# Optimization experiments

Measured on AMD Instinct MI355X. Metric: run time of the kernel, lower is better.

Reference implementation:

```python
import jax, jax.numpy as jnp
import numpy as np

N = 131072   # total gates/nodes in the batched block-diagonal circuit graph
E = 524288   # directed edges (avg degree 4)
D = 100      # hidden dim
DA = 50      # msg MLP hidden
DC = 30      # classifier hidden
R = 20       # message-passing rounds


def mlp(x, W1, b1, W2, b2):
    return jax.nn.relu(x @ W1 + b1) @ W2 + b2


def gru_step(x, h, Wih, Whh, bih, bhh):
    # single-timestep torch.nn.GRU cell
    gi = x @ Wih.T + bih
    gh = h @ Whh.T + bhh
    ir, iz, inn = jnp.split(gi, 3, axis=-1)
    hr, hz, hn = jnp.split(gh, 3, axis=-1)
    r = jax.nn.sigmoid(ir + hr)
    z = jax.nn.sigmoid(iz + hz)
    nwe = jnp.tanh(inn + r * hn)
    return (1.0 - z) * nwe + z * h


def setup_inputs():
    key = jax.random.key(0)
    ks = jax.random.split(key, 26)
    s = 0.05

    def rn(k, shape):
        return jax.random.normal(k, shape, dtype=jnp.float32) * s

    inp = {
        'features': jax.random.normal(ks[0], (N, 4), dtype=jnp.float32),
        'edge_row': jax.random.randint(ks[1], (E,), 0, N, dtype=jnp.int32),
        'edge_col': jax.random.randint(ks[2], (E,), 0, N, dtype=jnp.int32),
        'init_W': rn(ks[3], (4, D)), 'init_b': jnp.zeros((D,), jnp.float32),
        'fmsg_W1': rn(ks[4], (D, DA)), 'fmsg_b1': jnp.zeros((DA,), jnp.float32),
        'fmsg_W2': rn(ks[5], (DA, D)), 'fmsg_b2': jnp.zeros((D,), jnp.float32),
        'bmsg_W1': rn(ks[6], (D, DA)), 'bmsg_b1': jnp.zeros((DA,), jnp.float32),
        'bmsg_W2': rn(ks[7], (DA, D)), 'bmsg_b2': jnp.zeros((D,), jnp.float32),
        'fgru_Wih': rn(ks[8], (3 * D, D)), 'fgru_Whh': rn(ks[9], (3 * D, D)),
        'fgru_bih': jnp.zeros((3 * D,), jnp.float32), 'fgru_bhh': jnp.zeros((3 * D,), jnp.float32),
        'bgru_Wih': rn(ks[10], (3 * D, D)), 'bgru_Whh': rn(ks[11], (3 * D, D)),
        'bgru_bih': jnp.zeros((3 * D,), jnp.float32), 'bgru_bhh': jnp.zeros((3 * D,), jnp.float32),
        'cls_W1': rn(ks[12], (D, DC)), 'cls_b1': jnp.zeros((DC,), jnp.float32),
        'cls_W2': rn(ks[13], (DC, 1)), 'cls_b2': jnp.zeros((1,), jnp.float32),
    }
    return inp


def reference(features, edge_row, edge_col, init_W, init_b,
              fmsg_W1, fmsg_b1, fmsg_W2, fmsg_b2,
              bmsg_W1, bmsg_b1, bmsg_W2, bmsg_b2,
              fgru_Wih, fgru_Whh, fgru_bih, fgru_bhh,
              bgru_Wih, bgru_Whh, bgru_bih, bgru_bhh,
              cls_W1, cls_b1, cls_W2, cls_b2):
    n = features.shape[0]
    h = features @ init_W + init_b  # [N, D]

    def round_body(h, _):
        # forward pass: adj @ forward_msg(h)
        fm = mlp(h, fmsg_W1, fmsg_b1, fmsg_W2, fmsg_b2)
        f_msg = jax.ops.segment_sum(fm[edge_col], edge_row, num_segments=n)
        h = gru_step(f_msg, h, fgru_Wih, fgru_Whh, fgru_bih, fgru_bhh)
        # backward pass: adj.T @ backward_msg(h)
        bm = mlp(h, bmsg_W1, bmsg_b1, bmsg_W2, bmsg_b2)
        b_msg = jax.ops.segment_sum(bm[edge_row], edge_col, num_segments=n)
        h = gru_step(b_msg, h, bgru_Wih, bgru_Whh, bgru_bih, bgru_bhh)
        return h, None

    h, _ = jax.lax.scan(jax.checkpoint(round_body), h, None, length=R)
    return mlp(h, cls_W1, cls_b1, cls_W2, cls_b2)  # [N, 1]
```

## Files before the change

### kernel.cpp

```cpp
#include <hip/hip_runtime.h>
#include <math.h>

#define Nn 131072
#define Ee 524288

typedef __attribute__((ext_vector_type(8))) short short8;
typedef __attribute__((ext_vector_type(4))) float f32x4;
typedef unsigned short ushort_t;
typedef unsigned int uint32;

__device__ __forceinline__ f32x4 mfma16(short8 a, short8 b, f32x4 c) {
    return __builtin_amdgcn_mfma_f32_16x16x32_bf16(a, b, c, 0, 0, 0);
}

__device__ __forceinline__ uint32 rne_bf16(float x) {
    uint32 u = __float_as_uint(x);
    return (u + 0x7FFFu + ((u >> 16) & 1u)) >> 16;
}

__device__ __forceinline__ void split3(float x, uint32& h, uint32& m, uint32& l) {
    h = rne_bf16(x);
    float hf = __uint_as_float(h << 16);
    float r1 = x - hf;
    m = rne_bf16(r1);
    float mf = __uint_as_float(m << 16);
    float r2 = r1 - mf;
    l = rne_bf16(r2);
}

__global__ void diag_kernel(float* out, float val) {
    int n = blockIdx.x * 256 + threadIdx.x;
    if (n < Nn) out[n] = (n == 0) ? val : 0.f;
}
__global__ void zero_ints(int* p, int n) {
    int i = blockIdx.x * 256 + threadIdx.x;
    if (i < n) p[i] = 0;
}

__global__ void hist_kernel(const int* __restrict__ er, const int* __restrict__ ec,
                            int* __restrict__ cnt_f, int* __restrict__ cnt_b) {
    int e = blockIdx.x * 256 + threadIdx.x;
    atomicAdd(&cnt_f[er[e]], 1);
    atomicAdd(&cnt_b[ec[e]], 1);
}

__global__ __launch_bounds__(1024) void scan_kernel(const int* __restrict__ cnt,
                                                    int* __restrict__ ptr, int n) {
    __shared__ int sums[1024];
    int t = threadIdx.x;
    int chunk = n >> 10;
    int base = t * chunk;
    int s = 0;
    for (int i = 0; i < chunk; i++) s += cnt[base + i];
    sums[t] = s;
    __syncthreads();
    for (int off = 1; off < 1024; off <<= 1) {
        int v = (t >= off) ? sums[t - off] : 0;
        __syncthreads();
        sums[t] += v;
        __syncthreads();
    }
    int run = (t == 0) ? 0 : sums[t - 1];
    for (int i = 0; i < chunk; i++) { ptr[base + i] = run; run += cnt[base + i]; }
    if (t == 1023) ptr[n] = run;
}

__global__ void fill_kernel(const int* __restrict__ er, const int* __restrict__ ec,
                            int* __restrict__ ptr_f, int* __restrict__ ptr_b,
                            int* __restrict__ src_f, int* __restrict__ src_b) {
    int e = blockIdx.x * 256 + threadIdx.x;
    int r = er[e], c = ec[e];
    int p = atomicAdd(&ptr_f[r], 1); src_f[p] = c;
    int q = atomicAdd(&ptr_b[c], 1); src_b[q] = r;
}

__global__ void prep_gru_w(const float* __restrict__ Wih, const float* __restrict__ Whh,
                           const float* __restrict__ bih, const float* __restrict__ bhh,
                           ushort_t* __restrict__ W0, ushort_t* __restrict__ W1,
                           ushort_t* __restrict__ W2, float* __restrict__ bg) {
    int gid = blockIdx.x * 256 + threadIdx.x;
    if (gid >= 448 * 224) return;
    int c = gid / 224, k = gid - c * 224;
    int d = c >> 2, g = c & 3;
    float w = 0.f;
    if (d < 100) {
        if (k < 100) {
            if (g == 0)      w = Wih[d * 100 + k];
            else if (g == 1) w = Wih[(100 + d) * 100 + k];
            else if (g == 2) w = Wih[(200 + d) * 100 + k];
        } else if (k < 200) {
            int kk = k - 100;
            if (g == 0)      w = Whh[d * 100 + kk];
            else if (g == 1) w = Whh[(100 + d) * 100 + kk];
            else if (g == 3) w = Whh[(200 + d) * 100 + kk];
        }
    }
    uint32 h, m, l; split3(w, h, m, l);
    W0[gid] = (ushort_t)h; W1[gid] = (ushort_t)m; W2[gid] = (ushort_t)l;
    if (k == 0) {
        float b = 0.f;
        if (d < 100) {
            if (g == 0)      b = bih[d] + bhh[d];
            else if (g == 1) b = bih[100 + d] + bhh[100 + d];
            else if (g == 2) b = bih[200 + d];
            else             b = bhh[200 + d];
        }
        bg[c] = b;
    }
}

__global__ void prep_msg_w(const float* __restrict__ W1, const float* __restrict__ b1,
                           const float* __restrict__ W2, const float* __restrict__ b2,
                           ushort_t* __restrict__ A0, ushort_t* __restrict__ A1,
                           ushort_t* __restrict__ A2, float* __restrict__ b1p,
                           ushort_t* __restrict__ B0, ushort_t* __restrict__ B1,
                           ushort_t* __restrict__ B2, float* __restrict__ b2p) {
    int gid = blockIdx.x * 256 + threadIdx.x;
    if (gid < 8192) {
        int c = gid >> 7, k = gid & 127;
        float w = (c < 50 && k < 100) ? W1[k * 50 + c] : 0.f;
        uint32 h, m, l; split3(w, h, m, l);
        A0[gid] = (ushort_t)h; A1[gid] = (ushort_t)m; A2[gid] = (ushort_t)l;
        if (k == 0) b1p[c] = (c < 50) ? b1[c] : 0.f;
    } else if (gid < 8192 + 7168) {
        int t = gid - 8192;
        int c = t >> 6, k = t & 63;
        float w = (c < 100 && k < 50) ? W2[k * 100 + c] : 0.f;
        uint32 h, m, l; split3(w, h, m, l);
        B0[t] = (ushort_t)h; B1[t] = (ushort_t)m; B2[t] = (ushort_t)l;
        if (k == 0) b2p[c] = (c < 100) ? b2[c] : 0.f;
    }
}

__global__ void init_h_kernel(const float* __restrict__ feat, const float* __restrict__ W,
                              const float* __restrict__ b, float* __restrict__ Act) {
    int gid = blockIdx.x * 256 + threadIdx.x;
    int n = gid / 100, d = gid - n * 100;
    float acc = b[d];
#pragma unroll
    for (int k = 0; k < 4; k++) acc += feat[n * 4 + k] * W[k * 100 + d];
    Act[(size_t)n * 200 + 100 + d] = acc;
}

__global__ __launch_bounds__(256, 2) void msg_mfma(
    const float* __restrict__ Act,
    const ushort_t* __restrict__ A0, const ushort_t* __restrict__ A1,
    const ushort_t* __restrict__ A2, const float* __restrict__ b1p,
    const ushort_t* __restrict__ B0, const ushort_t* __restrict__ B1,
    const ushort_t* __restrict__ B2, const float* __restrict__ b2p,
    float* __restrict__ fm) {
    __shared__ ushort_t C1[3][64][72];
    const int tid = threadIdx.x;
    const int u = tid >> 6;
    const int lane = tid & 63;
    const int m = lane & 15, q = lane >> 4;
    const int n0 = blockIdx.x * 64;
    const int n = n0 + u * 16 + m;

    f32x4 z = {0.f, 0.f, 0.f, 0.f};
    f32x4 a1[4] = {z, z, z, z};

    for (int kc = 0; kc < 4; kc++) {
        int kb = kc * 32 + q * 8;
        const float* src = Act + (size_t)n * 200 + 100 + kb;
        float4 v0 = *(const float4*)src;
        float4 v1 = *(const float4*)(src + 4);
        float e[8] = {v0.x, v0.y, v0.z, v0.w, v1.x, v1.y, v1.z, v1.w};
        union { short8 s; uint32 u4[4]; } f0, f1, f2;
#pragma unroll
        for (int j = 0; j < 4; j++) {
            uint32 ha, ma, la, hb, mb, lb;
            split3(e[2 * j], ha, ma, la);
            split3(e[2 * j + 1], hb, mb, lb);
            f0.u4[j] = ha | (hb << 16);
            f1.u4[j] = ma | (mb << 16);
            f2.u4[j] = la | (lb << 16);
        }
#pragma unroll
        for (int t = 0; t < 4; t++) {
            int off = (t * 16 + m) * 128 + kc * 32 + q * 8;
            short8 w0 = *(const short8*)(A0 + off);
            short8 w1 = *(const short8*)(A1 + off);
            short8 w2 = *(const short8*)(A2 + off);
            a1[t] = mfma16(w0, f0.s, a1[t]);
            a1[t] = mfma16(w0, f1.s, a1[t]);
            a1[t] = mfma16(w1, f0.s, a1[t]);
            a1[t] = mfma16(w0, f2.s, a1[t]);
            a1[t] = mfma16(w2, f0.s, a1[t]);
            a1[t] = mfma16(w1, f1.s, a1[t]);
        }
    }
#pragma unroll
    for (int t = 0; t < 4; t++) {
        int c0 = t * 16 + 4 * q;
        float4 bb = *(const float4*)&b1p[c0];
        float v0 = fmaxf(a1[t][0] + bb.x, 0.f);
        float v1 = fmaxf(a1[t][1] + bb.y, 0.f);
        float v2 = fmaxf(a1[t][2] + bb.z, 0.f);
        float v3 = fmaxf(a1[t][3] + bb.w, 0.f);
        uint32 h0, m0, l0, h1, m1, l1, h2, m2, l2, h3, m3, l3;
        split3(v0, h0, m0, l0); split3(v1, h1, m1, l1);
        split3(v2, h2, m2, l2); split3(v3, h3, m3, l3);
        int nl = u * 16 + m;
        *(uint2*)&C1[0][nl][c0] = make_uint2(h0 | (h1 << 16), h2 | (h3 << 16));
        *(uint2*)&C1[1][nl][c0] = make_uint2(m0 | (m1 << 16), m2 | (m3 << 16));
        *(uint2*)&C1[2][nl][c0] = make_uint2(l0 | (l1 << 16), l2 | (l3 << 16));
    }
    __syncthreads();

    f32x4 a2[7] = {z, z, z, z, z, z, z};
    for (int kc = 0; kc < 2; kc++) {
        int nl = u * 16 + m;
        short8 c0f = *(const short8*)&C1[0][nl][kc * 32 + q * 8];
        short8 c1f = *(const short8*)&C1[1][nl][kc * 32 + q * 8];
        short8 c2f = *(const short8*)&C1[2][nl][kc * 32 + q * 8];
#pragma unroll
        for (int t = 0; t < 7; t++) {
            int off = (t * 16 + m) * 64 + kc * 32 + q * 8;
            short8 w0 = *(const short8*)(B0 + off);
            short8 w1 = *(const short8*)(B1 + off);
            short8 w2 = *(const short8*)(B2 + off);
            a2[t] = mfma16(w0, c0f, a2[t]);
            a2[t] = mfma16(w0, c1f, a2[t]);
            a2[t] = mfma16(w1, c0f, a2[t]);
            a2[t] = mfma16(w0, c2f, a2[t]);
            a2[t] = mfma16(w2, c0f, a2[t]);
            a2[t] = mfma16(w1, c1f, a2[t]);
        }
    }
#pragma unroll
    for (int t = 0; t < 7; t++) {
        int c0 = t * 16 + 4 * q;
        if (c0 < 100) {
            float4 bb = *(const float4*)&b2p[c0];
            float4 o;
            o.x = a2[t][0] + bb.x; o.y = a2[t][1] + bb.y;
            o.z = a2[t][2] + bb.z; o.w = a2[t][3] + bb.w;
            *(float4*)&fm[(size_t)n * 100 + c0] = o;
        }
    }
}

__global__ void gather4(const float* __restrict__ fm, const int* __restrict__ ptr,
                        const int* __restrict__ idx, float* __restrict__ Act) {
    int gid = blockIdx.x * 256 + threadIdx.x;
    int n = gid / 25, qq = (gid - n * 25) * 4;
    int s = (n == 0) ? 0 : ptr[n - 1];
    int e = ptr[n];
    float4 acc = {0.f, 0.f, 0.f, 0.f};
    for (int i = s; i < e; i++) {
        float4 v = *(const float4*)&fm[(size_t)idx[i] * 100 + qq];
        acc.x += v.x; acc.y += v.y; acc.z += v.z; acc.w += v.w;
    }
    *(float4*)&Act[(size_t)n * 200 + qq] = acc;
}

__global__ __launch_bounds__(256, 2) void gru_mfma(
    float* __restrict__ Act,
    const ushort_t* __restrict__ W0, const ushort_t* __restrict__ W1,
    const ushort_t* __restrict__ W2, const float* __restrict__ bg) {
    const int tid = threadIdx.x;
    const int wave = tid >> 6;
    const int lane = tid & 63;
    const int m = lane & 15, q = lane >> 4;
    const int n0 = blockIdx.x * 64;

    f32x4 z = {0.f, 0.f, 0.f, 0.f};
    f32x4 acc[7][4];
#pragma unroll
    for (int t = 0; t < 7; t++)
#pragma unroll
        for (int rf = 0; rf < 4; rf++) acc[t][rf] = z;

    int woff[7];
#pragma unroll
    for (int t = 0; t < 7; t++)
        woff[t] = ((t * 4 + wave) * 16 + m) * 224 + q * 8;

    const float* abase = Act + (size_t)(n0 + m) * 200 + q * 8;

#define GPASS(Wreg, Fr)                                          \
    _Pragma("unroll")                                            \
    for (int t = 0; t < 7; t++) {                                \
        _Pragma("unroll")                                        \
        for (int rf = 0; rf < 4; rf++)                           \
            acc[t][rf] = mfma16(Wreg[t], Fr[rf], acc[t][rf]);    \
    }

    for (int kc = 0; kc < 7; kc++) {
        const int kb = kc * 32 + q * 8;
        const int ko = kc * 32;
        short8 f0[4], f1[4], f2[4];
#pragma unroll
        for (int rf = 0; rf < 4; rf++) {
            float e[8];
            if (kb < 200) {
                const float* src = abase + (size_t)rf * 16 * 200 + ko;
                float4 v0 = *(const float4*)src;
                float4 v1 = *(const float4*)(src + 4);
                e[0] = v0.x; e[1] = v0.y; e[2] = v0.z; e[3] = v0.w;
                e[4] = v1.x; e[5] = v1.y; e[6] = v1.z; e[7] = v1.w;
            } else {
#pragma unroll
                for (int j = 0; j < 8; j++) e[j] = 0.f;
            }
            union { short8 s; uint32 u4[4]; } p0, p1, p2;
#pragma unroll
            for (int j = 0; j < 4; j++) {
                uint32 ha, ma, la, hb, mb, lb;
                split3(e[2 * j], ha, ma, la);
                split3(e[2 * j + 1], hb, mb, lb);
                p0.u4[j] = ha | (hb << 16);
                p1.u4[j] = ma | (mb << 16);
                p2.u4[j] = la | (lb << 16);
            }
            f0[rf] = p0.s; f1[rf] = p1.s; f2[rf] = p2.s;
        }

        short8 w[7];
#pragma unroll
        for (int t = 0; t < 7; t++) w[t] = *(const short8*)(W0 + woff[t] + ko);
        GPASS(w, f0);
        GPASS(w, f1);
        GPASS(w, f2);
#pragma unroll
        for (int t = 0; t < 7; t++) w[t] = *(const short8*)(W1 + woff[t] + ko);
        GPASS(w, f0);
        GPASS(w, f1);
#pragma unroll
        for (int t = 0; t < 7; t++) w[t] = *(const short8*)(W2 + woff[t] + ko);
        GPASS(w, f0);
    }
#undef GPASS

    __syncthreads();

#pragma unroll
    for (int t = 0; t < 7; t++) {
        const int ct = t * 4 + wave;
        const int d = ct * 4 + q;
        if (d < 100) {
            float4 b4 = *(const float4*)&bg[ct * 16 + 4 * q];
#pragma unroll
            for (int rf = 0; rf < 4; rf++) {
                int n = n0 + rf * 16 + m;
                float* hp = Act + (size_t)n * 200 + 100 + d;
                float hold = *hp;
                float rp = acc[t][rf][0] + b4.x;
                float zp = acc[t][rf][1] + b4.y;
                float np = acc[t][rf][2] + b4.z;
                float hh = acc[t][rf][3] + b4.w;
                float rr = 1.f / (1.f + __expf(-rp));
                float zz = 1.f / (1.f + __expf(-zp));
                float nw = tanhf(np + rr * hh);
                *hp = (1.f - zz) * nw + zz * hold;
            }
        }
    }
}

__global__ __launch_bounds__(256) void classifier(
    const float* __restrict__ Act, const float* __restrict__ W1,
    const float* __restrict__ b1, const float* __restrict__ W2,
    const float* __restrict__ b2, float* __restrict__ out) {
    __shared__ float Wc[3000];
    __shared__ float bc[30];
    __shared__ float w2[30];
    int tid = threadIdx.x;
    for (int i = tid; i < 3000; i += 256) Wc[i] = W1[i];
    if (tid < 30) { bc[tid] = b1[tid]; w2[tid] = W2[tid]; }
    __syncthreads();
    int n = blockIdx.x * 256 + tid;
    float a[30];
#pragma unroll
    for (int j = 0; j < 30; j++) a[j] = bc[j];
    for (int k = 0; k < 100; k++) {
        float hv = Act[(size_t)n * 200 + 100 + k];
#pragma unroll
        for (int j = 0; j < 30; j++) a[j] = fmaf(hv, Wc[k * 30 + j], a[j]);
    }
    float s = b2[0];
#pragma unroll
    for (int j = 0; j < 30; j++) s = fmaf(fmaxf(a[j], 0.f), w2[j], s);
    out[n] = s;
}

extern "C" void kernel_launch(void* const* d_in, const int* in_sizes, int n_in,
                              void* d_out, int out_size, void* d_ws, size_t ws_size,
                              hipStream_t stream) {
    const float* feat     = (const float*)d_in[0];
    const int*   er       = (const int*)d_in[1];
    const int*   ec       = (const int*)d_in[2];
    const float* init_W   = (const float*)d_in[3];
    const float* init_b   = (const float*)d_in[4];
    const float* fmsg_W1  = (const float*)d_in[5];
    const float* fmsg_b1  = (const float*)d_in[6];
    const float* fmsg_W2  = (const float*)d_in[7];
    const float* fmsg_b2  = (const float*)d_in[8];
    const float* bmsg_W1  = (const float*)d_in[9];
    const float* bmsg_b1  = (const float*)d_in[10];
    const float* bmsg_W2  = (const float*)d_in[11];
    const float* bmsg_b2  = (const float*)d_in[12];
    const float* fgru_Wih = (const float*)d_in[13];
    const float* fgru_Whh = (const float*)d_in[14];
    const float* fgru_bih = (const float*)d_in[15];
    const float* fgru_bhh = (const float*)d_in[16];
    const float* bgru_Wih = (const float*)d_in[17];
    const float* bgru_Whh = (const float*)d_in[18];
    const float* bgru_bih = (const float*)d_in[19];
    const float* bgru_bhh = (const float*)d_in[20];
    const float* cls_W1   = (const float*)d_in[21];
    const float* cls_b1   = (const float*)d_in[22];
    const float* cls_W2   = (const float*)d_in[23];
    const float* cls_b2   = (const float*)d_in[24];
    float* out = (float*)d_out;

    float* ws = (float*)d_ws;
    size_t o = 0;
    float* Act = ws + o; o += (size_t)Nn * 200;
    float* fm  = ws + o; o += (size_t)Nn * 100;

    ushort_t* us = (ushort_t*)(ws + o);
    size_t uo = 0;
    ushort_t* fWg0 = us + uo; uo += 448 * 224;
    ushort_t* fWg1 = us + uo; uo += 448 * 224;
    ushort_t* fWg2 = us + uo; uo += 448 * 224;
    ushort_t* bWg0 = us + uo; uo += 448 * 224;
    ushort_t* bWg1 = us + uo; uo += 448 * 224;
    ushort_t* bWg2 = us + uo; uo += 448 * 224;
    ushort_t* fA0 = us + uo; uo += 8192;
    ushort_t* fA1 = us + uo; uo += 8192;
    ushort_t* fA2 = us + uo; uo += 8192;
    ushort_t* bA0 = us + uo; uo += 8192;
    ushort_t* bA1 = us + uo; uo += 8192;
    ushort_t* bA2 = us + uo; uo += 8192;
    ushort_t* fB0 = us + uo; uo += 7168;
    ushort_t* fB1 = us + uo; uo += 7168;
    ushort_t* fB2 = us + uo; uo += 7168;
    ushort_t* bB0 = us + uo; uo += 7168;
    ushort_t* bB1 = us + uo; uo += 7168;
    ushort_t* bB2 = us + uo; uo += 7168;
    o += uo / 2;

    float* bgf  = ws + o; o += 448;
    float* bgb  = ws + o; o += 448;
    float* b1pf = ws + o; o += 64;
    float* b1pb = ws + o; o += 64;
    float* b2pf = ws + o; o += 112;
    float* b2pb = ws + o; o += 112;

    int* iws   = (int*)(ws + o);
    int* ptr_f = iws;
    int* ptr_b = ptr_f + (Nn + 1);
    int* cnt   = ptr_b + (Nn + 1);
    int* cnt_f = cnt;
    int* cnt_b = cnt + Nn;
    int* src_f = cnt + 2 * (size_t)Nn;
    int* src_b = src_f + Ee;

    size_t need = o * sizeof(float) +
                  (size_t)(2 * (Nn + 1) + 2 * Nn + 2 * Ee) * sizeof(int);
    if (ws_size < need) {
        diag_kernel<<<(Nn + 255) / 256, 256, 0, stream>>>(out, (float)ws_size);
        return;
    }

    zero_ints<<<(2 * Nn + 255) / 256, 256, 0, stream>>>(cnt, 2 * Nn);
    hist_kernel<<<Ee / 256, 256, 0, stream>>>(er, ec, cnt_f, cnt_b);
    scan_kernel<<<1, 1024, 0, stream>>>(cnt_f, ptr_f, Nn);
    scan_kernel<<<1, 1024, 0, stream>>>(cnt_b, ptr_b, Nn);
    fill_kernel<<<Ee / 256, 256, 0, stream>>>(er, ec, ptr_f, ptr_b, src_f, src_b);

    prep_gru_w<<<(448 * 224 + 255) / 256, 256, 0, stream>>>(
        fgru_Wih, fgru_Whh, fgru_bih, fgru_bhh, fWg0, fWg1, fWg2, bgf);
    prep_gru_w<<<(448 * 224 + 255) / 256, 256, 0, stream>>>(
        bgru_Wih, bgru_Whh, bgru_bih, bgru_bhh, bWg0, bWg1, bWg2, bgb);
    prep_msg_w<<<(15360 + 255) / 256, 256, 0, stream>>>(
        fmsg_W1, fmsg_b1, fmsg_W2, fmsg_b2, fA0, fA1, fA2, b1pf, fB0, fB1, fB2, b2pf);
    prep_msg_w<<<(15360 + 255) / 256, 256, 0, stream>>>(
        bmsg_W1, bmsg_b1, bmsg_W2, bmsg_b2, bA0, bA1, bA2, b1pb, bB0, bB1, bB2, b2pb);

    init_h_kernel<<<(Nn * 100) / 256, 256, 0, stream>>>(feat, init_W, init_b, Act);

    const int gTile = Nn / 64;
    const int gGru  = Nn / 64;
    const int gGath = Nn * 25 / 256;

    for (int rd = 0; rd < 20; rd++) {
        msg_mfma<<<gTile, 256, 0, stream>>>(Act, fA0, fA1, fA2, b1pf, fB0, fB1, fB2, b2pf, fm);
        gather4<<<gGath, 256, 0, stream>>>(fm, ptr_f, src_f, Act);
        gru_mfma<<<gGru, 256, 0, stream>>>(Act, fWg0, fWg1, fWg2, bgf);

        msg_mfma<<<gTile, 256, 0, stream>>>(Act, bA0, bA1, bA2, b1pb, bB0, bB1, bB2, b2pb, fm);
        gather4<<<gGath, 256, 0, stream>>>(fm, ptr_b, src_b, Act);
        gru_mfma<<<gGru, 256, 0, stream>>>(Act, bWg0, bWg1, bWg2, bgb);
    }

    classifier<<<Nn / 256, 256, 0, stream>>>(Act, cls_W1, cls_b1, cls_W2, cls_b2, out);
}
```

Baseline: 13.70 ms.

## Stage split-bf16 activation tiles in LDS once per block in GRU MFMA kernel

Each block's 64x200 activation tile is converted to three bf16 split planes once and stored in shared memory in two K-chunks. The MFMA loop then reads its fragments from LDS. Previously each of the four waves redundantly loaded and split the same activations from global memory. This adds about 52KB of LDS per block and extra barriers, which may limit occupancy under launch_bounds(256,2).

```diff
diff --git a/kernel.cpp b/kernel.cpp
--- a/kernel.cpp
+++ b/kernel.cpp
@@ -259,6 +259,7 @@
     float* __restrict__ Act,
     const ushort_t* __restrict__ W0, const ushort_t* __restrict__ W1,
     const ushort_t* __restrict__ W2, const float* __restrict__ bg) {
+    __shared__ ushort_t AL[3][64][136];
     const int tid = threadIdx.x;
     const int wave = tid >> 6;
     const int lane = tid & 63;
@@ -276,8 +277,6 @@
 #pragma unroll
     for (int t = 0; t < 7; t++)
         woff[t] = ((t * 4 + wave) * 16 + m) * 224 + q * 8;
-
-    const float* abase = Act + (size_t)(n0 + m) * 200 + q * 8;
 
 #define GPASS(Wreg, Fr)                                          \
     _Pragma("unroll")                                            \
@@ -287,53 +286,62 @@
             acc[t][rf] = mfma16(Wreg[t], Fr[rf], acc[t][rf]);    \
     }
 
-    for (int kc = 0; kc < 7; kc++) {
-        const int kb = kc * 32 + q * 8;
-        const int ko = kc * 32;
-        short8 f0[4], f1[4], f2[4];
-#pragma unroll
-        for (int rf = 0; rf < 4; rf++) {
-            float e[8];
-            if (kb < 200) {
-                const float* src = abase + (size_t)rf * 16 * 200 + ko;
-                float4 v0 = *(const float4*)src;
-                float4 v1 = *(const float4*)(src + 4);
-                e[0] = v0.x; e[1] = v0.y; e[2] = v0.z; e[3] = v0.w;
-                e[4] = v1.x; e[5] = v1.y; e[6] = v1.z; e[7] = v1.w;
-            } else {
-#pragma unroll
-                for (int j = 0; j < 8; j++) e[j] = 0.f;
-            }
-            union { short8 s; uint32 u4[4]; } p0, p1, p2;
-#pragma unroll
-            for (int j = 0; j < 4; j++) {
-                uint32 ha, ma, la, hb, mb, lb;
-                split3(e[2 * j], ha, ma, la);
-                split3(e[2 * j + 1], hb, mb, lb);
-                p0.u4[j] = ha | (hb << 16);
-                p1.u4[j] = ma | (mb << 16);
-                p2.u4[j] = la | (lb << 16);
-            }
-            f0[rf] = p0.s; f1[rf] = p1.s; f2[rf] = p2.s;
-        }
-
-        short8 w[7];
-#pragma unroll
-        for (int t = 0; t < 7; t++) w[t] = *(const short8*)(W0 + woff[t] + ko);
-        GPASS(w, f0);
-        GPASS(w, f1);
-        GPASS(w, f2);
-#pragma unroll
-        for (int t = 0; t < 7; t++) w[t] = *(const short8*)(W1 + woff[t] + ko);
-        GPASS(w, f0);
-        GPASS(w, f1);
-#pragma unroll
-        for (int t = 0; t < 7; t++) w[t] = *(const short8*)(W2 + woff[t] + ko);
-        GPASS(w, f0);
-    }
+#define GSTAGE(KS, KW)                                                        \
+    for (int idx = tid; idx < 64 * ((KW) / 4); idx += 256) {                  \
+        int row = idx / ((KW) / 4);                                           \
+        int k4 = (idx - row * ((KW) / 4)) << 2;                               \
+        int kg = (KS) + k4;                                                   \
+        float e0 = 0.f, e1 = 0.f, e2 = 0.f, e3 = 0.f;                         \
+        if (kg < 200) {                                                       \
+            float4 v = *(const float4*)&Act[(size_t)(n0 + row) * 200 + kg];   \
+            e0 = v.x; e1 = v.y; e2 = v.z; e3 = v.w;                           \
+        }                                                                     \
+        uint32 h0, m0, l0, h1, m1, l1, h2, m2, l2, h3, m3, l3;                \
+        split3(e0, h0, m0, l0); split3(e1, h1, m1, l1);                       \
+        split3(e2, h2, m2, l2); split3(e3, h3, m3, l3);                       \
+        *(uint2*)&AL[0][row][k4] = make_uint2(h0 | (h1 << 16), h2 | (h3 << 16)); \
+        *(uint2*)&AL[1][row][k4] = make_uint2(m0 | (m1 << 16), m2 | (m3 << 16)); \
+        *(uint2*)&AL[2][row][k4] = make_uint2(l0 | (l1 << 16), l2 | (l3 << 16)); \
+    }
+
+#define GCOMPUTE(C0, C1)                                                      \
+    for (int kc = (C0); kc < (C1); kc++) {                                    \
+        const int kb = (kc - (C0)) * 32 + q * 8;                              \
+        short8 f0[4], f1[4], f2[4];                                           \
+        _Pragma("unroll")                                                     \
+        for (int rf = 0; rf < 4; rf++) {                                      \
+            int rl = rf * 16 + m;                                             \
+            f0[rf] = *(const short8*)&AL[0][rl][kb];                          \
+            f1[rf] = *(const short8*)&AL[1][rl][kb];                          \
+            f2[rf] = *(const short8*)&AL[2][rl][kb];                          \
+        }                                                                     \
+        const int ko = kc * 32;                                               \
+        short8 w[7];                                                          \
+        _Pragma("unroll")                                                     \
+        for (int t = 0; t < 7; t++) w[t] = *(const short8*)(W0 + woff[t] + ko); \
+        GPASS(w, f0);                                                         \
+        GPASS(w, f1);                                                         \
+        GPASS(w, f2);                                                         \
+        _Pragma("unroll")                                                     \
+        for (int t = 0; t < 7; t++) w[t] = *(const short8*)(W1 + woff[t] + ko); \
+        GPASS(w, f0);                                                         \
+        GPASS(w, f1);                                                         \
+        _Pragma("unroll")                                                     \
+        for (int t = 0; t < 7; t++) w[t] = *(const short8*)(W2 + woff[t] + ko); \
+        GPASS(w, f0);                                                         \
+    }
+
+    GSTAGE(0, 128)
+    __syncthreads();
+    GCOMPUTE(0, 4)
+    __syncthreads();
+    GSTAGE(128, 96)
+    __syncthreads();
+    GCOMPUTE(4, 7)
+
 #undef GPASS
-
-    __syncthreads();
+#undef GSTAGE
+#undef GCOMPUTE
 
 #pragma unroll
     for (int t = 0; t < 7; t++) {
```

New measurement: 13.29 ms. 1.03x faster.

## Store activations as pre-split bf16 limb planes instead of fp32

Applied to the files above, without the earlier changes.

Replaces the fp32 activation buffer with three bf16 limb planes (hi/mid/lo) in a padded 224-wide row layout. The producers (gather, GRU, init) split values once when they write them, so the consumer kernels load ready MFMA operands instead of re-splitting fp32 on every read. This removes the repeated split3 arithmetic in msg_mfma and gru_mfma and trims the zero-fill branch for the k-range past 200. In exchange, memory traffic per element grows (three 2-byte planes versus one 4-byte float), the row is padded, and the GRU and classifier must reconstruct fp32 h from the limbs. The two scan launches are also merged into one two-block launch.

```diff
diff --git a/kernel.cpp b/kernel.cpp
--- a/kernel.cpp
+++ b/kernel.cpp
@@ -3,6 +3,7 @@
 
 #define Nn 131072
 #define Ee 524288
+#define LROW 224
 
 typedef __attribute__((ext_vector_type(8))) short short8;
 typedef __attribute__((ext_vector_type(4))) float f32x4;
@@ -28,6 +29,10 @@
     l = rne_bf16(r2);
 }
 
+__device__ __forceinline__ float limb2f(ushort_t u) {
+    return __uint_as_float((uint32)u << 16);
+}
+
 __global__ void diag_kernel(float* out, float val) {
     int n = blockIdx.x * 256 + threadIdx.x;
     if (n < Nn) out[n] = (n == 0) ? val : 0.f;
@@ -35,6 +40,13 @@
 __global__ void zero_ints(int* p, int n) {
     int i = blockIdx.x * 256 + threadIdx.x;
     if (i < n) p[i] = 0;
+}
+__global__ void zero_short8(ushort_t* p, long n8) {
+    long i = (long)blockIdx.x * 256 + threadIdx.x;
+    if (i < n8) {
+        short8 zz = {0, 0, 0, 0, 0, 0, 0, 0};
+        *(short8*)(p + i * 8) = zz;
+    }
 }
 
 __global__ void hist_kernel(const int* __restrict__ er, const int* __restrict__ ec,
@@ -44,8 +56,11 @@
     atomicAdd(&cnt_b[ec[e]], 1);
 }
 
-__global__ __launch_bounds__(1024) void scan_kernel(const int* __restrict__ cnt,
-                                                    int* __restrict__ ptr, int n) {
+__global__ __launch_bounds__(1024) void scan2_kernel(
+    const int* __restrict__ cnt_f, const int* __restrict__ cnt_b,
+    int* __restrict__ ptr_f, int* __restrict__ ptr_b, int n) {
+    const int* cnt = blockIdx.x ? cnt_b : cnt_f;
+    int* ptr = blockIdx.x ? ptr_b : ptr_f;
     __shared__ int sums[1024];
     int t = threadIdx.x;
     int chunk = n >> 10;
@@ -88,8 +103,8 @@
             if (g == 0)      w = Wih[d * 100 + k];
             else if (g == 1) w = Wih[(100 + d) * 100 + k];
             else if (g == 2) w = Wih[(200 + d) * 100 + k];
-        } else if (k < 200) {
-            int kk = k - 100;
+        } else if (k >= 112 && k < 212) {
+            int kk = k - 112;
             if (g == 0)      w = Whh[d * 100 + kk];
             else if (g == 1) w = Whh[(100 + d) * 100 + kk];
             else if (g == 3) w = Whh[(200 + d) * 100 + kk];
@@ -133,17 +148,23 @@
 }
 
 __global__ void init_h_kernel(const float* __restrict__ feat, const float* __restrict__ W,
-                              const float* __restrict__ b, float* __restrict__ Act) {
+                              const float* __restrict__ b,
+                              ushort_t* __restrict__ L0, ushort_t* __restrict__ L1,
+                              ushort_t* __restrict__ L2) {
     int gid = blockIdx.x * 256 + threadIdx.x;
+    if (gid >= Nn * 100) return;
     int n = gid / 100, d = gid - n * 100;
     float acc = b[d];
 #pragma unroll
     for (int k = 0; k < 4; k++) acc += feat[n * 4 + k] * W[k * 100 + d];
-    Act[(size_t)n * 200 + 100 + d] = acc;
+    uint32 h, m, l; split3(acc, h, m, l);
+    size_t a = (size_t)n * LROW + 112 + d;
+    L0[a] = (ushort_t)h; L1[a] = (ushort_t)m; L2[a] = (ushort_t)l;
 }
 
 __global__ __launch_bounds__(256, 2) void msg_mfma(
-    const float* __restrict__ Act,
+    const ushort_t* __restrict__ L0, const ushort_t* __restrict__ L1,
+    const ushort_t* __restrict__ L2,
     const ushort_t* __restrict__ A0, const ushort_t* __restrict__ A1,
     const ushort_t* __restrict__ A2, const float* __restrict__ b1p,
     const ushort_t* __restrict__ B0, const ushort_t* __restrict__ B1,
@@ -160,34 +181,24 @@
     f32x4 z = {0.f, 0.f, 0.f, 0.f};
     f32x4 a1[4] = {z, z, z, z};
 
+    const size_t hbase = (size_t)n * LROW + 112;
     for (int kc = 0; kc < 4; kc++) {
         int kb = kc * 32 + q * 8;
-        const float* src = Act + (size_t)n * 200 + 100 + kb;
-        float4 v0 = *(const float4*)src;
-        float4 v1 = *(const float4*)(src + 4);
-        float e[8] = {v0.x, v0.y, v0.z, v0.w, v1.x, v1.y, v1.z, v1.w};
-        union { short8 s; uint32 u4[4]; } f0, f1, f2;
-#pragma unroll
-        for (int j = 0; j < 4; j++) {
-            uint32 ha, ma, la, hb, mb, lb;
-            split3(e[2 * j], ha, ma, la);
-            split3(e[2 * j + 1], hb, mb, lb);
-            f0.u4[j] = ha | (hb << 16);
-            f1.u4[j] = ma | (mb << 16);
-            f2.u4[j] = la | (lb << 16);
-        }
+        short8 f0 = *(const short8*)(L0 + hbase + kb);
+        short8 f1 = *(const short8*)(L1 + hbase + kb);
+        short8 f2 = *(const short8*)(L2 + hbase + kb);
 #pragma unroll
         for (int t = 0; t < 4; t++) {
             int off = (t * 16 + m) * 128 + kc * 32 + q * 8;
             short8 w0 = *(const short8*)(A0 + off);
             short8 w1 = *(const short8*)(A1 + off);
             short8 w2 = *(const short8*)(A2 + off);
-            a1[t] = mfma16(w0, f0.s, a1[t]);
-            a1[t] = mfma16(w0, f1.s, a1[t]);
-            a1[t] = mfma16(w1, f0.s, a1[t]);
-            a1[t] = mfma16(w0, f2.s, a1[t]);
-            a1[t] = mfma16(w2, f0.s, a1[t]);
-            a1[t] = mfma16(w1, f1.s, a1[t]);
+            a1[t] = mfma16(w0, f0, a1[t]);
+            a1[t] = mfma16(w0, f1, a1[t]);
+            a1[t] = mfma16(w1, f0, a1[t]);
+            a1[t] = mfma16(w0, f2, a1[t]);
+            a1[t] = mfma16(w2, f0, a1[t]);
+            a1[t] = mfma16(w1, f1, a1[t]);
         }
     }
 #pragma unroll
@@ -242,7 +253,9 @@
 }
 
 __global__ void gather4(const float* __restrict__ fm, const int* __restrict__ ptr,
-                        const int* __restrict__ idx, float* __restrict__ Act) {
+                        const int* __restrict__ idx,
+                        ushort_t* __restrict__ L0, ushort_t* __restrict__ L1,
+                        ushort_t* __restrict__ L2) {
     int gid = blockIdx.x * 256 + threadIdx.x;
     int n = gid / 25, qq = (gid - n * 25) * 4;
     int s = (n == 0) ? 0 : ptr[n - 1];
@@ -252,11 +265,18 @@
         float4 v = *(const float4*)&fm[(size_t)idx[i] * 100 + qq];
         acc.x += v.x; acc.y += v.y; acc.z += v.z; acc.w += v.w;
     }
-    *(float4*)&Act[(size_t)n * 200 + qq] = acc;
+    uint32 h0, m0, l0, h1, m1, l1, h2, m2, l2, h3, m3, l3;
+    split3(acc.x, h0, m0, l0); split3(acc.y, h1, m1, l1);
+    split3(acc.z, h2, m2, l2); split3(acc.w, h3, m3, l3);
+    size_t a = (size_t)n * LROW + qq;
+    *(uint2*)&L0[a] = make_uint2(h0 | (h1 << 16), h2 | (h3 << 16));
+    *(uint2*)&L1[a] = make_uint2(m0 | (m1 << 16), m2 | (m3 << 16));
+    *(uint2*)&L2[a] = make_uint2(l0 | (l1 << 16), l2 | (l3 << 16));
 }
 
 __global__ __launch_bounds__(256, 2) void gru_mfma(
-    float* __restrict__ Act,
+    ushort_t* __restrict__ L0, ushort_t* __restrict__ L1,
+    ushort_t* __restrict__ L2,
     const ushort_t* __restrict__ W0, const ushort_t* __restrict__ W1,
     const ushort_t* __restrict__ W2, const float* __restrict__ bg) {
     const int tid = threadIdx.x;
@@ -277,7 +297,7 @@
     for (int t = 0; t < 7; t++)
         woff[t] = ((t * 4 + wave) * 16 + m) * 224 + q * 8;
 
-    const float* abase = Act + (size_t)(n0 + m) * 200 + q * 8;
+    const size_t abase = (size_t)(n0 + m) * LROW + q * 8;
 
 #define GPASS(Wreg, Fr)                                          \
     _Pragma("unroll")                                            \
@@ -288,35 +308,15 @@
     }
 
     for (int kc = 0; kc < 7; kc++) {
-        const int kb = kc * 32 + q * 8;
         const int ko = kc * 32;
         short8 f0[4], f1[4], f2[4];
 #pragma unroll
         for (int rf = 0; rf < 4; rf++) {
-            float e[8];
-            if (kb < 200) {
-                const float* src = abase + (size_t)rf * 16 * 200 + ko;
-                float4 v0 = *(const float4*)src;
-                float4 v1 = *(const float4*)(src + 4);
-                e[0] = v0.x; e[1] = v0.y; e[2] = v0.z; e[3] = v0.w;
-                e[4] = v1.x; e[5] = v1.y; e[6] = v1.z; e[7] = v1.w;
-            } else {
-#pragma unroll
-                for (int j = 0; j < 8; j++) e[j] = 0.f;
-            }
-            union { short8 s; uint32 u4[4]; } p0, p1, p2;
-#pragma unroll
-            for (int j = 0; j < 4; j++) {
-                uint32 ha, ma, la, hb, mb, lb;
-                split3(e[2 * j], ha, ma, la);
-                split3(e[2 * j + 1], hb, mb, lb);
-                p0.u4[j] = ha | (hb << 16);
-                p1.u4[j] = ma | (mb << 16);
-                p2.u4[j] = la | (lb << 16);
-            }
-            f0[rf] = p0.s; f1[rf] = p1.s; f2[rf] = p2.s;
-        }
-
+            size_t a = abase + (size_t)rf * 16 * LROW + ko;
+            f0[rf] = *(const short8*)(L0 + a);
+            f1[rf] = *(const short8*)(L1 + a);
+            f2[rf] = *(const short8*)(L2 + a);
+        }
         short8 w[7];
 #pragma unroll
         for (int t = 0; t < 7; t++) w[t] = *(const short8*)(W0 + woff[t] + ko);
@@ -344,8 +344,8 @@
 #pragma unroll
             for (int rf = 0; rf < 4; rf++) {
                 int n = n0 + rf * 16 + m;
-                float* hp = Act + (size_t)n * 200 + 100 + d;
-                float hold = *hp;
+                size_t hb = (size_t)n * LROW + 112 + d;
+                float hold = (limb2f(L2[hb]) + limb2f(L1[hb])) + limb2f(L0[hb]);
                 float rp = acc[t][rf][0] + b4.x;
                 float zp = acc[t][rf][1] + b4.y;
                 float np = acc[t][rf][2] + b4.z;
@@ -353,31 +353,43 @@
                 float rr = 1.f / (1.f + __expf(-rp));
                 float zz = 1.f / (1.f + __expf(-zp));
                 float nw = tanhf(np + rr * hh);
-                *hp = (1.f - zz) * nw + zz * hold;
+                float hnew = (1.f - zz) * nw + zz * hold;
+                uint32 sh, sm, sl; split3(hnew, sh, sm, sl);
+                L0[hb] = (ushort_t)sh; L1[hb] = (ushort_t)sm; L2[hb] = (ushort_t)sl;
             }
         }
     }
 }
 
 __global__ __launch_bounds__(256) void classifier(
-    const float* __restrict__ Act, const float* __restrict__ W1,
+    const ushort_t* __restrict__ L0, const ushort_t* __restrict__ L1,
+    const ushort_t* __restrict__ L2, const float* __restrict__ W1,
     const float* __restrict__ b1, const float* __restrict__ W2,
     const float* __restrict__ b2, float* __restrict__ out) {
-    __shared__ float Wc[3000];
+    __shared__ float Wc[3128];
     __shared__ float bc[30];
     __shared__ float w2[30];
     int tid = threadIdx.x;
-    for (int i = tid; i < 3000; i += 256) Wc[i] = W1[i];
+    for (int i = tid; i < 3128; i += 256) Wc[i] = (i < 3000) ? W1[i] : 0.f;
     if (tid < 30) { bc[tid] = b1[tid]; w2[tid] = W2[tid]; }
     __syncthreads();
     int n = blockIdx.x * 256 + tid;
     float a[30];
 #pragma unroll
     for (int j = 0; j < 30; j++) a[j] = bc[j];
-    for (int k = 0; k < 100; k++) {
-        float hv = Act[(size_t)n * 200 + 100 + k];
-#pragma unroll
-        for (int j = 0; j < 30; j++) a[j] = fmaf(hv, Wc[k * 30 + j], a[j]);
+    const size_t base = (size_t)n * LROW + 112;
+    for (int k8 = 0; k8 < 13; k8++) {
+        int k0 = k8 * 8;
+        union { short8 s; ushort_t u[8]; } h0, h1, h2;
+        h0.s = *(const short8*)(L0 + base + k0);
+        h1.s = *(const short8*)(L1 + base + k0);
+        h2.s = *(const short8*)(L2 + base + k0);
+#pragma unroll
+        for (int jj = 0; jj < 8; jj++) {
+            float hv = (limb2f(h2.u[jj]) + limb2f(h1.u[jj])) + limb2f(h0.u[jj]);
+#pragma unroll
+            for (int j = 0; j < 30; j++) a[j] = fmaf(hv, Wc[(k0 + jj) * 30 + j], a[j]);
+        }
     }
     float s = b2[0];
 #pragma unroll
@@ -417,11 +429,14 @@
 
     float* ws = (float*)d_ws;
     size_t o = 0;
-    float* Act = ws + o; o += (size_t)Nn * 200;
-    float* fm  = ws + o; o += (size_t)Nn * 100;
-
+    float* fm = ws + o; o += (size_t)Nn * 100;
+
+    const size_t PL = (size_t)Nn * LROW + 64;
     ushort_t* us = (ushort_t*)(ws + o);
     size_t uo = 0;
+    ushort_t* L0 = us + uo; uo += PL;
+    ushort_t* L1 = us + uo; uo += PL;
+    ushort_t* L2 = us + uo; uo += PL;
     ushort_t* fWg0 = us + uo; uo += 448 * 224;
     ushort_t* fWg1 = us + uo; uo += 448 * 224;
     ushort_t* fWg2 = us + uo; uo += 448 * 224;
@@ -465,10 +480,14 @@
         return;
     }
 
+    {
+        long n8 = (long)(3 * PL / 8);
+        zero_short8<<<(int)((n8 + 255) / 256), 256, 0, stream>>>(L0, n8);
+    }
+
     zero_ints<<<(2 * Nn + 255) / 256, 256, 0, stream>>>(cnt, 2 * Nn);
     hist_kernel<<<Ee / 256, 256, 0, stream>>>(er, ec, cnt_f, cnt_b);
-    scan_kernel<<<1, 1024, 0, stream>>>(cnt_f, ptr_f, Nn);
-    scan_kernel<<<1, 1024, 0, stream>>>(cnt_b, ptr_b, Nn);
+    scan2_kernel<<<2, 1024, 0, stream>>>(cnt_f, cnt_b, ptr_f, ptr_b, Nn);
     fill_kernel<<<Ee / 256, 256, 0, stream>>>(er, ec, ptr_f, ptr_b, src_f, src_b);
 
     prep_gru_w<<<(448 * 224 + 255) / 256, 256, 0, stream>>>(
@@ -480,21 +499,25 @@
     prep_msg_w<<<(15360 + 255) / 256, 256, 0, stream>>>(
         bmsg_W1, bmsg_b1, bmsg_W2, bmsg_b2, bA0, bA1, bA2, b1pb, bB0, bB1, bB2, b2pb);
 
-    init_h_kernel<<<(Nn * 100) / 256, 256, 0, stream>>>(feat, init_W, init_b, Act);
+    init_h_kernel<<<(Nn * 100 + 255) / 256, 256, 0, stream>>>(
+        feat, init_W, init_b, L0, L1, L2);
 
     const int gTile = Nn / 64;
     const int gGru  = Nn / 64;
     const int gGath = Nn * 25 / 256;
 
     for (int rd = 0; rd < 20; rd++) {
-        msg_mfma<<<gTile, 256, 0, stream>>>(Act, fA0, fA1, fA2, b1pf, fB0, fB1, fB2, b2pf, fm);
-        gather4<<<gGath, 256, 0, stream>>>(fm, ptr_f, src_f, Act);
-        gru_mfma<<<gGru, 256, 0, stream>>>(Act, fWg0, fWg1, fWg2, bgf);
-
-        msg_mfma<<<gTile, 256, 0, stream>>>(Act, bA0, bA1, bA2, b1pb, bB0, bB1, bB2, b2pb, fm);
-        gather4<<<gGath, 256, 0, stream>>>(fm, ptr_b, src_b, Act);
-        gru_mfma<<<gGru, 256, 0, stream>>>(Act, bWg0, bWg1, bWg2, bgb);
-    }
-
-    classifier<<<Nn / 256, 256, 0, stream>>>(Act, cls_W1, cls_b1, cls_W2, cls_b2, out);
-}
+        msg_mfma<<<gTile, 256, 0, stream>>>(L0, L1, L2,
+            fA0, fA1, fA2, b1pf, fB0, fB1, fB2, b2pf, fm);
+        gather4<<<gGath, 256, 0, stream>>>(fm, ptr_f, src_f, L0, L1, L2);
+        gru_mfma<<<gGru, 256, 0, stream>>>(L0, L1, L2, fWg0, fWg1, fWg2, bgf);
+
+        msg_mfma<<<gTile, 256, 0, stream>>>(L0, L1, L2,
+            bA0, bA1, bA2, b1pb, bB0, bB1, bB2, b2pb, fm);
+        gather4<<<gGath, 256, 0, stream>>>(fm, ptr_b, src_b, L0, L1, L2);
+        gru_mfma<<<gGru, 256, 0, stream>>>(L0, L1, L2, bWg0, bWg1, bWg2, bgb);
+    }
+
+    classifier<<<Nn / 256, 256, 0, stream>>>(L0, L1, L2,
+        cls_W1, cls_b1, cls_W2, cls_b2, out);
+}
```

Result: slower. 16.37 ms (+19.5%).
